# Kernel optimization log

Hardware: AMD Instinct MI355X
Metric: run time of the kernel (lower is better)

Reference implementation:

```python
import jax, jax.numpy as jnp
import numpy as np

NU, NI, E, D, B, L = 100000, 50000, 800000, 64, 1024, 2
P_DROP, TEMP = 0.25, 0.2
L1, L2, L3 = 0.2, 0.01, 1e-5


def setup_inputs() -> dict:
    k = jax.random.split(jax.random.key(0), 20)
    s = 0.02  # xavier-ish scale for embedding tables
    return dict(
        E_u_0=jax.random.normal(k[0], (NU, D), jnp.float32) * s,
        E_i_0=jax.random.normal(k[1], (NI, D), jnp.float32) * s,
        fuse_w=jax.random.normal(k[2], (E,), jnp.float32),
        fuse_b=jax.random.normal(k[3], (E,), jnp.float32),
        W1u=jax.random.normal(k[4], (D, D), jnp.float32) / np.sqrt(D),
        W1i=jax.random.normal(k[5], (D, D), jnp.float32) / np.sqrt(D),
        b1=jnp.zeros((D,), jnp.float32),
        W2=jax.random.normal(k[6], (D,), jnp.float32) / np.sqrt(D),
        b2=jnp.zeros((1,), jnp.float32),
        att_a=jax.random.normal(k[7], (2 * D,), jnp.float32) / np.sqrt(2 * D),
        wv_param=jax.random.normal(k[8], (E,), jnp.float32),
        Wg=jax.random.normal(k[9], (D, D), jnp.float32) / np.sqrt(D),
        adj_vals=jax.random.uniform(k[10], (E,), jnp.float32, 0.001, 0.02),
        drop_main_u=jax.random.uniform(k[11], (2 * L, E), jnp.float32),
        drop_aug_u=jax.random.uniform(k[12], (2 * L, E), jnp.float32),
        edge_src=jax.random.randint(k[13], (E,), 0, NU),
        edge_dst=jax.random.randint(k[14], (E,), 0, NI),
        uids=jax.random.randint(k[15], (B,), 0, NU),
        iids=jax.random.randint(k[16], (B,), 0, NI),
        pos_ids=jax.random.randint(k[17], (B,), 0, NI),
        neg_ids=jax.random.randint(k[18], (B,), 0, NI),
    )


def _forward(E_u_0, E_i_0, fuse_w, fuse_b, W1u, W1i, b1, W2, b2, att_a,
             wv_param, Wg, adj_vals, drop_main_u, drop_aug_u,
             edge_src, edge_dst, uids, iids, pos_ids, neg_ids):
    dt = adj_vals.dtype

    def spmm_u(vals, Xi):  # A @ Xi -> [NU, D]
        return jax.ops.segment_sum(vals[:, None] * Xi[edge_dst], edge_src, num_segments=NU)

    def spmm_i(vals, Xu):  # A.T @ Xu -> [NI, D]
        return jax.ops.segment_sum(vals[:, None] * Xu[edge_src], edge_dst, num_segments=NI)

    def mask(u):  # sparse_dropout: keep w.p. 1-p, rescale
        return (u > P_DROP).astype(dt) / (1.0 - P_DROP)

    def propagate(vals, drops):  # LightGCN-style sum over layers
        Eu, Ei = E_u_0, E_i_0
        Su, Si = Eu, Ei
        for layer in range(L):
            Eu_n = spmm_u(vals * mask(drops[2 * layer]), Ei)
            Ei_n = spmm_i(vals * mask(drops[2 * layer + 1]), Eu)
            Eu, Ei = Eu_n, Ei_n
            Su, Si = Su + Eu, Si + Ei
        return Su, Si

    E_u, E_i = propagate(adj_vals, drop_main_u)

    eu0, ei0 = E_u_0[edge_src], E_i_0[edge_dst]  # [E, D]
    # MLP view
    h = jax.nn.relu(eu0 @ W1u + ei0 @ W1i + b1)
    Ag_mlp = jax.nn.sigmoid(h @ W2 + b2[0])
    # WV view: learnable per-edge weight
    Ag_wv = jax.nn.sigmoid(wv_param)
    # GCN view: one propagation on current embeddings, bilinear edge score
    h_u = spmm_u(adj_vals, E_i)
    h_i = spmm_i(adj_vals, E_u)
    Ag_gcn = jax.nn.sigmoid(jnp.sum((h_u[edge_src] @ Wg) * h_i[edge_dst], axis=1))
    # ATT view: GAT-style
    Ag_att = jax.nn.sigmoid(jax.nn.leaky_relu(eu0 @ att_a[:D] + ei0 @ att_a[D:], 0.2))

    views = jnp.stack([Ag_mlp, Ag_wv, Ag_gcn, Ag_att])  # [4, E]
    w = jax.nn.softmax(jnp.tanh(fuse_w * views + fuse_b), axis=1)  # softmax over edges (as in source)
    Ag = jnp.sum(w * views, axis=0)
    Ag = (Ag + (views - Ag).sum(0)) / 5.0  # mlp_cof = 1 -> (sum(views) - 3*Ag) / 5

    # refine: sigmoid of endpoint dot products
    pre = jax.nn.sigmoid(jnp.sum(E_u[edge_src] * E_i[edge_dst], axis=1))
    baew = pre * Ag  # batch_aug_edge_weight

    aug_vals = jax.lax.stop_gradient(baew) * adj_vals  # new_graph * adj_norm (detach + Hadamard)
    Z_u, Z_i = propagate(aug_vals, drop_aug_u)

    # contrastive loss
    Gu, Gi = Z_u[uids], Z_i[iids]
    neg_sc = jnp.log(jnp.exp(Gu @ E_u.T / TEMP).sum(1) + 1e-8).mean() \
           + jnp.log(jnp.exp(Gi @ E_i.T / TEMP).sum(1) + 1e-8).mean()
    pos_sc = jnp.clip((Gu * E_u[uids]).sum(1) / TEMP, -5.0, 5.0).mean() \
           + jnp.clip((Gi * E_i[iids]).sum(1) / TEMP, -5.0, 5.0).mean()
    loss_cl = -pos_sc + neg_sc

    # BPR loss
    u_e, p_e, n_e = E_u[uids], E_i[pos_ids], E_i[neg_ids]
    diff = (u_e * p_e).sum(-1) - (u_e * n_e).sum(-1)
    loss_bpr = -jnp.log(jax.nn.sigmoid(diff)).mean()

    loss_pr = L2 * (-jnp.log(baew)).mean()

    params = [E_u_0, E_i_0, fuse_w, fuse_b, W1u, W1i, b1, W2, b2, att_a, wv_param, Wg]
    loss_reg = L3 * sum((p_ ** 2).sum() for p_ in params)

    loss = loss_bpr + L1 * loss_cl + loss_pr + loss_reg
    return loss, loss_bpr, L1 * loss_cl, loss_pr


def reference(E_u_0, E_i_0, fuse_w, fuse_b, W1u, W1i, b1, W2, b2, att_a,
              wv_param, Wg, adj_vals, drop_main_u, drop_aug_u,
              edge_src, edge_dst, uids, iids, pos_ids, neg_ids):
    return _forward(E_u_0, E_i_0, fuse_w, fuse_b, W1u, W1i, b1, W2, b2, att_a,
                    wv_param, Wg, adj_vals, drop_main_u, drop_aug_u,
                    edge_src, edge_dst, uids, iids, pos_ids, neg_ids)
```

## Files before the change

### kernel.cpp

```cpp
#include <hip/hip_runtime.h>
#include <math.h>

constexpr int NUc = 100000;
constexpr int NIc = 50000;
constexpr int Ec  = 800000;
constexpr int Bc  = 1024;

typedef __attribute__((ext_vector_type(8))) short short8;
typedef __attribute__((ext_vector_type(8))) unsigned short ushort8;
typedef __attribute__((ext_vector_type(4))) unsigned short ushort4v;
typedef __attribute__((ext_vector_type(4))) float floatx4;

__device__ __forceinline__ float sigf(float x) { return 1.f / (1.f + __expf(-x)); }
__device__ __forceinline__ float maskf(float u) { return (u > 0.25f) ? (1.f / 0.75f) : 0.f; }
__device__ __forceinline__ unsigned short f2bf(float f) {
    unsigned int u = __float_as_uint(f);
    unsigned int r = (u + 0x7fffu + ((u >> 16) & 1u)) >> 16;
    return (unsigned short)r;
}
__device__ __forceinline__ float bf2f(unsigned short u) {
    return __uint_as_float((unsigned int)u << 16);
}

__global__ void hist_k(const int* __restrict__ idx, int* __restrict__ cnt, int n) {
    int i = blockIdx.x * blockDim.x + threadIdx.x;
    if (i < n) atomicAdd(&cnt[idx[i]], 1);
}

__global__ void scan_block(const int* __restrict__ cnt, int* __restrict__ rp,
                           int* __restrict__ bsum, int N) {
    __shared__ int sh[1024];
    int i = blockIdx.x * 1024 + threadIdx.x;
    int v = (i < N) ? cnt[i] : 0;
    sh[threadIdx.x] = v;
    __syncthreads();
    for (int off = 1; off < 1024; off <<= 1) {
        int t = (threadIdx.x >= off) ? sh[threadIdx.x - off] : 0;
        __syncthreads();
        sh[threadIdx.x] += t;
        __syncthreads();
    }
    if (i < N) rp[i + 1] = sh[threadIdx.x];
    if (threadIdx.x == 1023) bsum[blockIdx.x] = sh[1023];
}

__global__ void scan_bsums(int* __restrict__ bsum, int nb) {
    __shared__ int sh[128];
    int t = threadIdx.x;
    int v = (t < nb) ? bsum[t] : 0;
    sh[t] = v;
    __syncthreads();
    for (int off = 1; off < 128; off <<= 1) {
        int x = (t >= off) ? sh[t - off] : 0;
        __syncthreads();
        sh[t] += x;
        __syncthreads();
    }
    if (t < nb) bsum[t] = sh[t] - v;
}

__global__ void scan_add(const int* __restrict__ bsum, int* __restrict__ rp, int N) {
    int i = blockIdx.x * blockDim.x + threadIdx.x;
    if (i == 0) rp[0] = 0;
    if (i < N) rp[i + 1] += bsum[i >> 10];
}

__global__ void fill_csr(const int* __restrict__ key, const int* __restrict__ other,
                         int* __restrict__ cur, int* __restrict__ col,
                         int* __restrict__ pos, int* __restrict__ perm, int n) {
    int i = blockIdx.x * blockDim.x + threadIdx.x;
    if (i < n) {
        int r = key[i];
        int p = atomicAdd(&cur[r], 1);
        col[p] = other[i];
        pos[i] = p;
        perm[p] = i;
    }
}

__global__ void build_rowu(const int* __restrict__ rp, int* __restrict__ rowu, int N) {
    int r = blockIdx.x * blockDim.x + threadIdx.x;
    if (r < N) {
        int s = rp[r], e = rp[r + 1];
        for (int p = s; p < e; ++p) rowu[p] = r;
    }
}

__global__ void build_w_gather(const int* __restrict__ perm, const float* __restrict__ vals,
                               const float* __restrict__ dA, const float* __restrict__ dB,
                               float* __restrict__ outA, float* __restrict__ outB, int E) {
    int p = blockIdx.x * blockDim.x + threadIdx.x;
    if (p >= E) return;
    int e = perm[p];
    float a = vals[e];
    outA[p] = a * maskf(dA[e]);
    outB[p] = a * maskf(dB[e]);
}

__global__ void gather_vals(const int* __restrict__ perm, const float* __restrict__ vals,
                            float* __restrict__ outA, int E) {
    int p = blockIdx.x * blockDim.x + threadIdx.x;
    if (p >= E) return;
    outA[p] = vals[perm[p]];
}

__global__ void spmm_bf(const int* __restrict__ rp, const int* __restrict__ col,
                        const float* __restrict__ w, const unsigned short* __restrict__ Xbf,
                        float* __restrict__ Acc, const float* __restrict__ Base,
                        unsigned short* __restrict__ Ybf, int ystride, int yoff, int N) {
    int row = blockIdx.x * (blockDim.x >> 6) + (threadIdx.x >> 6);
    int lane = threadIdx.x & 63;
    if (row >= N) return;
    int s = rp[row], e = rp[row + 1];
    float acc = 0.f;
    int j = s;
    for (; j + 4 <= e; j += 4) {
        int c0 = col[j], c1 = col[j + 1], c2 = col[j + 2], c3 = col[j + 3];
        float w0 = w[j], w1 = w[j + 1], w2 = w[j + 2], w3 = w[j + 3];
        float x0 = bf2f(Xbf[(size_t)c0 * 64 + lane]);
        float x1 = bf2f(Xbf[(size_t)c1 * 64 + lane]);
        float x2 = bf2f(Xbf[(size_t)c2 * 64 + lane]);
        float x3 = bf2f(Xbf[(size_t)c3 * 64 + lane]);
        acc = fmaf(w0, x0, acc);
        acc = fmaf(w1, x1, acc);
        acc = fmaf(w2, x2, acc);
        acc = fmaf(w3, x3, acc);
    }
    for (; j < e; ++j) acc = fmaf(w[j], bf2f(Xbf[(size_t)col[j] * 64 + lane]), acc);
    size_t o = (size_t)row * 64 + lane;
    if (Acc) Acc[o] = (Base ? Base[o] : Acc[o]) + acc;
    if (Ybf) Ybf[(size_t)row * ystride + yoff + lane] = f2bf(acc);
}

__global__ void gemm_n64_bf(const unsigned short* __restrict__ Xbf, const float* __restrict__ W,
                            unsigned short* __restrict__ P, int ostride, int ooff, int N) {
    __shared__ float Wl[64 * 64];
    for (int i = threadIdx.x; i < 4096; i += blockDim.x) Wl[i] = W[i];
    __syncthreads();
    int wid = blockIdx.x * (blockDim.x >> 6) + (threadIdx.x >> 6);
    int lane = threadIdx.x & 63;
    for (int r = 0; r < 8; ++r) {
        int row = wid * 8 + r;
        if (row >= N) break;
        const unsigned short* xr = Xbf + (size_t)row * 64;
        float acc = 0.f;
#pragma unroll
        for (int k = 0; k < 64; ++k) acc = fmaf(bf2f(xr[k]), Wl[k * 64 + lane], acc);
        P[(size_t)row * ostride + ooff + lane] = f2bf(acc);
    }
}

__global__ void rowdot64(const float* __restrict__ X, const float* __restrict__ a,
                         float* __restrict__ out, int N) {
    int wid = blockIdx.x * (blockDim.x >> 6) + (threadIdx.x >> 6);
    int lane = threadIdx.x & 63;
    float av = a[lane];
    for (int r = 0; r < 8; ++r) {
        int row = wid * 8 + r;
        if (row >= N) break;
        float v = X[(size_t)row * 64 + lane] * av;
#pragma unroll
        for (int off = 32; off; off >>= 1) v += __shfl_xor(v, off, 64);
        if (lane == 0) out[row] = v;
    }
}

__global__ void cvt_bf16(const float4* __restrict__ X, ushort4* __restrict__ Y, int n4) {
    int i = blockIdx.x * blockDim.x + threadIdx.x;
    if (i < n4) {
        float4 v = X[i];
        Y[i] = make_ushort4(f2bf(v.x), f2bf(v.y), f2bf(v.z), f2bf(v.w));
    }
}

__global__ void cvt_pack4(const float4* __restrict__ X, unsigned short* __restrict__ P,
                          int ostride, int ooff, int N) {
    int t = blockIdx.x * blockDim.x + threadIdx.x;
    if (t >= N * 16) return;
    int node = t >> 4, q = t & 15;
    float4 v = X[t];
    ushort4* dst = (ushort4*)(P + (size_t)node * ostride + ooff);
    dst[q] = make_ushort4(f2bf(v.x), f2bf(v.y), f2bf(v.z), f2bf(v.w));
}

__global__ void pack_bf4(const ushort4* __restrict__ X, unsigned short* __restrict__ P,
                         int ostride, int ooff, int N) {
    int t = blockIdx.x * blockDim.x + threadIdx.x;
    if (t >= N * 16) return;
    int node = t >> 4, q = t & 15;
    ((ushort4*)(P + (size_t)node * ostride + ooff))[q] = X[t];
}

__global__ void __launch_bounds__(128) edge_pass1(
        const int* __restrict__ rowu, const int* __restrict__ colP,
        const unsigned short* __restrict__ PU, const unsigned short* __restrict__ PI,
        const float* __restrict__ b1, const float* __restrict__ W2,
        const float* __restrict__ b2,
        const float* __restrict__ auv, const float* __restrict__ aiv,
        float4* __restrict__ vp4, int E) {
    __shared__ ushort4v lds4[128 * 49];
    int p0 = blockIdx.x * 128;
    int tid = threadIdx.x;
#pragma unroll
    for (int it = 0; it < 24; ++it) {
        int flat = it * 128 + tid;
        int row = flat / 24, c = flat - row * 24;
        int d = colP[p0 + row];
        ushort8 g = *(const ushort8*)(PI + (size_t)d * 192 + c * 8);
        ushort4v lo = {g[0], g[1], g[2], g[3]};
        ushort4v hi = {g[4], g[5], g[6], g[7]};
        lds4[row * 49 + c * 2]     = lo;
        lds4[row * 49 + c * 2 + 1] = hi;
    }
    __syncthreads();
    int p = p0 + tid;
    int s = rowu[p];
    int d = colP[p];
    const ushort8* pu = (const ushort8*)(PU + (size_t)s * 192);
    const ushort4v* pl = lds4 + tid * 49;
    float r1 = 0.f, r2 = 0.f, r3 = 0.f;
#pragma unroll
    for (int k = 0; k < 8; ++k) {
        ushort8 u1 = pu[k], hu = pu[8 + k], su = pu[16 + k];
// ... 59 lines not shown
        atomicAdd(&sumexp[threadIdx.x],
                  sh[0][threadIdx.x] + sh[1][threadIdx.x] + sh[2][threadIdx.x] + sh[3][threadIdx.x]);
}

__global__ void edge_pass2b(const float4* __restrict__ viewsE, const float* __restrict__ preE,
                            const float* __restrict__ fw, const float* __restrict__ fb,
                            const float* __restrict__ adj, const float* __restrict__ sumexp,
                            float* __restrict__ av, float* __restrict__ neglog, int E) {
    int e = blockIdx.x * blockDim.x + threadIdx.x;
    float nl = 0.f;
    if (e < E) {
        float s0 = sumexp[0], s1 = sumexp[1], s2 = sumexp[2], s3 = sumexp[3];
        float4 v = viewsE[e];
        float fwe = fw[e], fbe = fb[e];
        float w0 = __expf(tanhf(fmaf(fwe, v.x, fbe))) / s0;
        float w1 = __expf(tanhf(fmaf(fwe, v.y, fbe))) / s1;
        float w2 = __expf(tanhf(fmaf(fwe, v.z, fbe))) / s2;
        float w3 = __expf(tanhf(fmaf(fwe, v.w, fbe))) / s3;
        float agw = w0 * v.x + w1 * v.y + w2 * v.z + w3 * v.w;
        float sv = v.x + v.y + v.z + v.w;
        float Ag = (sv - 3.f * agw) * 0.2f;
        float bw = preE[e] * Ag;
        av[e] = bw * adj[e];
        nl = -logf(bw);
    }
#pragma unroll
    for (int off = 32; off; off >>= 1) nl += __shfl_xor(nl, off, 64);
    __shared__ float sh4[4];
    if ((threadIdx.x & 63) == 0) sh4[threadIdx.x >> 6] = nl;
    __syncthreads();
    if (threadIdx.x == 0) atomicAdd(neglog, sh4[0] + sh4[1] + sh4[2] + sh4[3]);
}

__global__ void gather_cvt(const float* __restrict__ X, const int* __restrict__ ids,
                           unsigned short* __restrict__ Y, int B_) {
    int t = blockIdx.x * blockDim.x + threadIdx.x;
    if (t >= B_ * 64) return;
    int b = t >> 6, k = t & 63;
    Y[t] = f2bf(X[(size_t)ids[b] * 64 + k]);
}

__global__ void lse_mfma(const unsigned short* __restrict__ Gbf,
                         const unsigned short* __restrict__ Ebf,
                         float* __restrict__ sums, int N, int tilesPerChunk) {
    int wid = blockIdx.x * (blockDim.x >> 6) + (threadIdx.x >> 6);
    int lane = threadIdx.x & 63;
    int bgroup = wid & 15;
    int chunk = wid >> 4;
    int ntiles = N >> 4;
    int t0 = chunk * tilesPerChunk;
    if (t0 >= ntiles) return;
    int t1 = t0 + tilesPerChunk; if (t1 > ntiles) t1 = ntiles;
    int m = lane & 15, quad = lane >> 4;

    short8 a0[4], a1[4];
#pragma unroll
    for (int t = 0; t < 4; ++t) {
        const short8* ap = (const short8*)(Gbf + ((size_t)(bgroup * 64 + t * 16 + m)) * 64 + quad * 8);
        a0[t] = ap[0];
        a1[t] = ap[4];
    }
    floatx4 rs[4];
#pragma unroll
    for (int t = 0; t < 4; ++t) rs[t] = (floatx4){0.f, 0.f, 0.f, 0.f};

    for (int jt = t0; jt < t1; ++jt) {
        const short8* bp = (const short8*)(Ebf + ((size_t)(jt * 16 + m)) * 64 + quad * 8);
        short8 bf0 = bp[0], bf1 = bp[4];
#pragma unroll
        for (int t = 0; t < 4; ++t) {
            floatx4 c = (floatx4){0.f, 0.f, 0.f, 0.f};
            c = __builtin_amdgcn_mfma_f32_16x16x32_bf16(a0[t], bf0, c, 0, 0, 0);
            c = __builtin_amdgcn_mfma_f32_16x16x32_bf16(a1[t], bf1, c, 0, 0, 0);
#pragma unroll
            for (int r = 0; r < 4; ++r) rs[t][r] += __expf(c[r] * 5.f);
        }
    }
#pragma unroll
    for (int t = 0; t < 4; ++t) {
#pragma unroll
        for (int r = 0; r < 4; ++r) {
            float v = rs[t][r];
            v += __shfl_xor(v, 1, 64);
            v += __shfl_xor(v, 2, 64);
            v += __shfl_xor(v, 4, 64);
            v += __shfl_xor(v, 8, 64);
            if (m == 0) atomicAdd(&sums[bgroup * 64 + t * 16 + quad * 4 + r], v);
        }
    }
}

__global__ void sumsq(const float* __restrict__ x, int n, float* __restrict__ acc) {
    float s = 0.f;
    for (int i = blockIdx.x * blockDim.x + threadIdx.x; i < n; i += gridDim.x * blockDim.x) {
        float v = x[i];
        s = fmaf(v, v, s);
    }
#pragma unroll
    for (int off = 32; off; off >>= 1) s += __shfl_xor(s, off, 64);
    __shared__ float sh[4];
    if ((threadIdx.x & 63) == 0) sh[threadIdx.x >> 6] = s;
    __syncthreads();
    if (threadIdx.x == 0) atomicAdd(acc, sh[0] + sh[1] + sh[2] + sh[3]);
}

__global__ void batch_partial(const float* __restrict__ Su, const float* __restrict__ Si,
                              const float* __restrict__ Zu, const float* __restrict__ Zi,
                              const int* __restrict__ uids, const int* __restrict__ iids,
                              const int* __restrict__ pids, const int* __restrict__ nids,
                              float* __restrict__ pos_b, float* __restrict__ bpr_b) {
    int b = blockIdx.x * (blockDim.x >> 6) + (threadIdx.x >> 6);
    if (b >= Bc) return;
    int lane = threadIdx.x & 63;
    int u = uids[b], ii = iids[b], p = pids[b], n = nids[b];
    float zu = Zu[(size_t)u * 64 + lane],  su = Su[(size_t)u * 64 + lane];
    float zi = Zi[(size_t)ii * 64 + lane], si = Si[(size_t)ii * 64 + lane];
    float pe = Si[(size_t)p * 64 + lane],  ne = Si[(size_t)n * 64 + lane];
    float du = zu * su, di = zi * si, dp = su * pe, dn = su * ne;
#pragma unroll
    for (int off = 32; off; off >>= 1) {
        du += __shfl_xor(du, off, 64);
        di += __shfl_xor(di, off, 64);
        dp += __shfl_xor(dp, off, 64);
        dn += __shfl_xor(dn, off, 64);
    }
    if (lane == 0) {
        pos_b[b] = fminf(fmaxf(du * 5.f, -5.f), 5.f) + fminf(fmaxf(di * 5.f, -5.f), 5.f);
        bpr_b[b] = log1pf(__expf(-(dp - dn)));
    }
}

__global__ void finalize_kernel(const float* __restrict__ sumexp_u, const float* __restrict__ sumexp_i,
                                const float* __restrict__ pos_b, const float* __restrict__ bpr_b,
                                const float* __restrict__ neglog, const float* __restrict__ regsum,
                                float* __restrict__ out) {
    int b = threadIdx.x;
    float lse = logf(sumexp_u[b] + 1e-8f) + logf(sumexp_i[b] + 1e-8f);
    float pos = pos_b[b];
    float bpr = bpr_b[b];
#pragma unroll
    for (int off = 32; off; off >>= 1) {
        lse += __shfl_xor(lse, off, 64);
        pos += __shfl_xor(pos, off, 64);
        bpr += __shfl_xor(bpr, off, 64);
    }
    __shared__ float sl[16], sp[16], sb[16];
    int w = b >> 6;
    if ((b & 63) == 0) { sl[w] = lse; sp[w] = pos; sb[w] = bpr; }
    __syncthreads();
    if (b == 0) {
        float L = 0.f, P = 0.f, Bz = 0.f;
        for (int i = 0; i < 16; ++i) { L += sl[i]; P += sp[i]; Bz += sb[i]; }
        float neg_sc = L * (1.f / Bc);
        float pos_sc = P * (1.f / Bc);
        float loss_cl = neg_sc - pos_sc;
        float l1cl = 0.2f * loss_cl;
        float loss_bpr = Bz * (1.f / Bc);
        float loss_pr = 0.01f * (neglog[0] * (1.f / Ec));
        float loss_reg = 1e-5f * regsum[0];
        out[0] = loss_bpr + l1cl + loss_pr + loss_reg;
        out[1] = loss_bpr;
        out[2] = l1cl;
// ... 39 lines not shown
    char* blkZ = alloc((size_t)NUc * 64 * 4 + (size_t)NIc * 64 * 4);
    unsigned short* PU = (unsigned short*)blkZ;
    float4* viewsE = (float4*)blkZ;
    float* preE   = (float*)(blkZ + (size_t)Ec * 16);
    float* Zu = (float*)blkZ;
    float* Zi = (float*)(blkZ + (size_t)NUc * 64 * 4);
    float4* vp4 = (float4*)alloc((size_t)Ec * 16);
    unsigned short* Eu0bf = (unsigned short*)alloc((size_t)NUc * 64 * 2);
    unsigned short* Ei0bf = (unsigned short*)alloc((size_t)NIc * 64 * 2);
    unsigned short* Subf  = (unsigned short*)alloc((size_t)NUc * 64 * 2);
    unsigned short* Sibf  = (unsigned short*)alloc((size_t)NIc * 64 * 2);
    unsigned short* Bubf  = (unsigned short*)alloc((size_t)NUc * 64 * 2);
    unsigned short* Bibf  = (unsigned short*)alloc((size_t)NIc * 64 * 2);
    unsigned short* hubf  = (unsigned short*)alloc((size_t)NUc * 64 * 2);
    unsigned short* hibf  = (unsigned short*)alloc((size_t)NIc * 64 * 2);
    char* blkA = alloc((size_t)Ec * 4 * 6);
    float* adjPu = (float*)blkA;
    float* adjPi = (float*)(blkA + (size_t)Ec * 4);
    float* wAu0  = (float*)(blkA + (size_t)Ec * 8);
    float* wAu1  = (float*)(blkA + (size_t)Ec * 12);
    float* wAi0  = (float*)(blkA + (size_t)Ec * 16);
    float* wAi1  = (float*)(blkA + (size_t)Ec * 20);
    unsigned short* PI = (unsigned short*)blkA;
    float* wMu0  = (float*)alloc((size_t)Ec * 4);
    float* wMu1  = (float*)alloc((size_t)Ec * 4);
    float* wMi0  = (float*)alloc((size_t)Ec * 4);
    float* wMi1  = (float*)alloc((size_t)Ec * 4);
    float* av    = (float*)alloc((size_t)Ec * 4);
    float* auv  = (float*)alloc((size_t)NUc * 4);
    float* aiv  = (float*)alloc((size_t)NIc * 4);
    int* rowu  = (int*)alloc((size_t)Ec * 4);
    unsigned short* Gubf = (unsigned short*)alloc((size_t)Bc * 64 * 2);
    unsigned short* Gibf = (unsigned short*)alloc((size_t)Bc * 64 * 2);
    float* sumexp4 = (float*)alloc(4 * 4);
    float* neglog  = (float*)alloc(4);
    float* regsum  = (float*)alloc(4);
    float* sumexp_u= (float*)alloc((size_t)Bc * 4);
    float* sumexp_i= (float*)alloc((size_t)Bc * 4);
    float* pos_b   = (float*)alloc((size_t)Bc * 4);
    float* bpr_b   = (float*)alloc((size_t)Bc * 4);
    int* rpu   = (int*)alloc((size_t)(NUc + 1) * 4);
    int* rpi   = (int*)alloc((size_t)(NIc + 1) * 4);
    int* colu  = (int*)alloc((size_t)Ec * 4);
    int* coli  = (int*)alloc((size_t)Ec * 4);
    int* posu  = (int*)alloc((size_t)Ec * 4);
    int* posi  = (int*)alloc((size_t)Ec * 4);
    int* permu = (int*)alloc((size_t)Ec * 4);
    int* permi = (int*)alloc((size_t)Ec * 4);
    int* cnt   = (int*)alloc((size_t)NUc * 4);
    int* cur   = (int*)alloc((size_t)NUc * 4);
    int* bsum  = (int*)alloc(128 * 4);

    dim3 b256(256);
    const int nbU = (NUc + 1023) / 1024;
    const int nbI = (NIc + 1023) / 1024;
    const dim3 gE((Ec + 255) / 256);
    const dim3 gU((NUc + 3) / 4), gI((NIc + 3) / 4);
    const dim3 gU8((NUc + 31) / 32), gI8((NIc + 31) / 32);
    const dim3 gUp((NUc * 16 + 255) / 256), gIp((NIc * 16 + 255) / 256);

    hipMemsetAsync(cnt, 0, (size_t)NUc * 4, stream);
    hist_k<<<gE, b256, 0, stream>>>(esrc, cnt, Ec);
    scan_block<<<dim3(nbU), dim3(1024), 0, stream>>>(cnt, rpu, bsum, NUc);
    scan_bsums<<<dim3(1), dim3(128), 0, stream>>>(bsum, nbU);
    scan_add<<<dim3((NUc + 255) / 256), b256, 0, stream>>>(bsum, rpu, NUc);
    hipMemcpyAsync(cur, rpu, (size_t)NUc * 4, hipMemcpyDeviceToDevice, stream);
    fill_csr<<<gE, b256, 0, stream>>>(esrc, edst, cur, colu, posu, permu, Ec);
    build_rowu<<<dim3((NUc + 255) / 256), b256, 0, stream>>>(rpu, rowu, NUc);

    hipMemsetAsync(cnt, 0, (size_t)NIc * 4, stream);
    hist_k<<<gE, b256, 0, stream>>>(edst, cnt, Ec);
    scan_block<<<dim3(nbI), dim3(1024), 0, stream>>>(cnt, rpi, bsum, NIc);
    scan_bsums<<<dim3(1), dim3(128), 0, stream>>>(bsum, nbI);
    scan_add<<<dim3((NIc + 255) / 256), b256, 0, stream>>>(bsum, rpi, NIc);
    hipMemcpyAsync(cur, rpi, (size_t)NIc * 4, hipMemcpyDeviceToDevice, stream);
    fill_csr<<<gE, b256, 0, stream>>>(edst, esrc, cur, coli, posi, permi, Ec);

    build_w_gather<<<gE, b256, 0, stream>>>(permu, adj, dmain, dmain + 2 * (size_t)Ec, wMu0, wMu1, Ec);
    build_w_gather<<<gE, b256, 0, stream>>>(permi, adj, dmain + (size_t)Ec, dmain + 3 * (size_t)Ec, wMi0, wMi1, Ec);
    gather_vals<<<gE, b256, 0, stream>>>(permu, adj, adjPu, Ec);
    gather_vals<<<gE, b256, 0, stream>>>(permi, adj, adjPi, Ec);

    cvt_bf16<<<gUp, b256, 0, stream>>>((const float4*)Eu0, (ushort4*)Eu0bf, NUc * 16);
    cvt_bf16<<<gIp, b256, 0, stream>>>((const float4*)Ei0, (ushort4*)Ei0bf, NIc * 16);

    spmm_bf<<<gU, b256, 0, stream>>>(rpu, colu, wMu0, Ei0bf, Su, Eu0, Bubf, 64, 0, NUc);
    spmm_bf<<<gI, b256, 0, stream>>>(rpi, coli, wMi0, Eu0bf, Si, Ei0, Bibf, 64, 0, NIc);
    spmm_bf<<<gU, b256, 0, stream>>>(rpu, colu, wMu1, Bibf, Su, nullptr, nullptr, 64, 0, NUc);
    spmm_bf<<<gI, b256, 0, stream>>>(rpi, coli, wMi1, Bubf, Si, nullptr, nullptr, 64, 0, NIc);

    cvt_bf16<<<gUp, b256, 0, stream>>>((const float4*)Su, (ushort4*)Subf, NUc * 16);
    cvt_bf16<<<gIp, b256, 0, stream>>>((const float4*)Si, (ushort4*)Sibf, NIc * 16);

    spmm_bf<<<gU, b256, 0, stream>>>(rpu, colu, adjPu, Sibf, nullptr, nullptr, hubf, 64, 0, NUc);
    spmm_bf<<<gI, b256, 0, stream>>>(rpi, coli, adjPi, Subf, nullptr, nullptr, hibf, 64, 0, NIc);
    gemm_n64_bf<<<gU8, b256, 0, stream>>>(hubf, Wg, PU, 192, 64, NUc);
    gemm_n64_bf<<<gU8, b256, 0, stream>>>(Eu0bf, W1u, PU, 192, 0, NUc);
    gemm_n64_bf<<<gI8, b256, 0, stream>>>(Ei0bf, W1i, PI, 192, 0, NIc);
    pack_bf4<<<gIp, b256, 0, stream>>>((const ushort4*)hibf, PI, 192, 64, NIc);
    cvt_pack4<<<gUp, b256, 0, stream>>>((const float4*)Su, PU, 192, 128, NUc);
    cvt_pack4<<<gIp, b256, 0, stream>>>((const float4*)Si, PI, 192, 128, NIc);

    rowdot64<<<gU8, b256, 0, stream>>>(Eu0, att, auv, NUc);
    rowdot64<<<gI8, b256, 0, stream>>>(Ei0, att + 64, aiv, NIc);

    edge_pass1<<<dim3(Ec / 128), dim3(128), 0, stream>>>(
        rowu, colu, PU, PI, b1, W2, b2, auv, aiv, vp4, Ec);

    hipMemsetAsync(sumexp4, 0, 4 * 4, stream);
    edge_pass2a<<<gE, b256, 0, stream>>>(vp4, posu, fuse_w, fuse_b, wv,
                                         viewsE, preE, sumexp4, Ec);

    hipMemsetAsync(neglog, 0, 4, stream);
    edge_pass2b<<<gE, b256, 0, stream>>>(
        viewsE, preE, fuse_w, fuse_b, adj, sumexp4, av, neglog, Ec);

    build_w_gather<<<gE, b256, 0, stream>>>(permu, av, daug, daug + 2 * (size_t)Ec, wAu0, wAu1, Ec);
    build_w_gather<<<gE, b256, 0, stream>>>(permi, av, daug + (size_t)Ec, daug + 3 * (size_t)Ec, wAi0, wAi1, Ec);

    spmm_bf<<<gU, b256, 0, stream>>>(rpu, colu, wAu0, Ei0bf, Zu, Eu0, Bubf, 64, 0, NUc);
    spmm_bf<<<gI, b256, 0, stream>>>(rpi, coli, wAi0, Eu0bf, Zi, Ei0, Bibf, 64, 0, NIc);
    spmm_bf<<<gU, b256, 0, stream>>>(rpu, colu, wAu1, Bibf, Zu, nullptr, nullptr, 64, 0, NUc);
    spmm_bf<<<gI, b256, 0, stream>>>(rpi, coli, wAi1, Bubf, Zi, nullptr, nullptr, 64, 0, NIc);

    gather_cvt<<<dim3((Bc * 64 + 255) / 256), b256, 0, stream>>>(Zu, uids, Gubf, Bc);
    gather_cvt<<<dim3((Bc * 64 + 255) / 256), b256, 0, stream>>>(Zi, iids, Gibf, Bc);
    hipMemsetAsync(sumexp_u, 0, (size_t)Bc * 4, stream);
    hipMemsetAsync(sumexp_i, 0, (size_t)Bc * 4, stream);
    lse_mfma<<<dim3(640), b256, 0, stream>>>(Gubf, Subf, sumexp_u, NUc, 40);
    lse_mfma<<<dim3(320), b256, 0, stream>>>(Gibf, Sibf, sumexp_i, NIc, 40);

    batch_partial<<<dim3(Bc / 4), b256, 0, stream>>>(Su, Si, Zu, Zi, uids, iids, pids, nids,
                                                     pos_b, bpr_b);

    hipMemsetAsync(regsum, 0, 4, stream);
    auto ss = [&](const float* p, int n) {
        int g = (n + 2047) / 2048;
        if (g > 1024) g = 1024;
        if (g < 1) g = 1;
        sumsq<<<dim3(g), b256, 0, stream>>>(p, n, regsum);
    };
    ss(Eu0, NUc * 64); ss(Ei0, NIc * 64); ss(fuse_w, Ec); ss(fuse_b, Ec);
    ss(W1u, 4096); ss(W1i, 4096); ss(b1, 64); ss(W2, 64); ss(b2, 1);
    ss(att, 128); ss(wv, Ec); ss(Wg, 4096);

    finalize_kernel<<<dim3(1), dim3(1024), 0, stream>>>(
        sumexp_u, sumexp_i, pos_b, bpr_b, neglog, regsum, out);
}
```

Measured before the change: 1.368 ms.

## Merge user/item kernel pairs and fuse prep stages to cut launch count

Builds both CSR structures from one histogram, one scan and one fill pass, and merges the user and item SpMM, weight-build, conversion, gather and log-sum-exp kernels into single launches that split work by block index. The two GEMMs, the attention row-dots and the packing into PU/PI are folded into per-side prep kernels, and bf16 copies of Su/Si are written inside the SpMM. The twelve sumsq launches and several memsets are collapsed into one kernel and one memset. The aim is to cut launch overhead and redundant memory passes, at the cost of larger kernels with more shared memory per block in prep_PU.

After: 1.253 ms. 8.4% less time.

```diff
diff --git a/kernel.cpp b/kernel.cpp
--- a/kernel.cpp
+++ b/kernel.cpp
@@ -22,12 +22,16 @@
     return __uint_as_float((unsigned int)u << 16);
 }
 
-__global__ void hist_k(const int* __restrict__ idx, int* __restrict__ cnt, int n) {
+__global__ void hist_both(const int* __restrict__ esrc, const int* __restrict__ edst,
+                          int* __restrict__ cntAll, int n) {
     int i = blockIdx.x * blockDim.x + threadIdx.x;
-    if (i < n) atomicAdd(&cnt[idx[i]], 1);
-}
-
-__global__ void scan_block(const int* __restrict__ cnt, int* __restrict__ rp,
+    if (i < n) {
+        atomicAdd(&cntAll[esrc[i]], 1);
+        atomicAdd(&cntAll[NUc + edst[i]], 1);
+    }
+}
+
+__global__ void scan_block(const int* __restrict__ cnt, int* __restrict__ scanAll,
                            int* __restrict__ bsum, int N) {
     __shared__ int sh[1024];
     int i = blockIdx.x * 1024 + threadIdx.x;
@@ -40,17 +44,17 @@
         sh[threadIdx.x] += t;
         __syncthreads();
     }
-    if (i < N) rp[i + 1] = sh[threadIdx.x];
+    if (i < N) scanAll[i] = sh[threadIdx.x];
     if (threadIdx.x == 1023) bsum[blockIdx.x] = sh[1023];
 }
 
 __global__ void scan_bsums(int* __restrict__ bsum, int nb) {
-    __shared__ int sh[128];
+    __shared__ int sh[256];
     int t = threadIdx.x;
     int v = (t < nb) ? bsum[t] : 0;
     sh[t] = v;
     __syncthreads();
-    for (int off = 1; off < 128; off <<= 1) {
+    for (int off = 1; off < 256; off <<= 1) {
         int x = (t >= off) ? sh[t - off] : 0;
         __syncthreads();
         sh[t] += x;
@@ -59,23 +63,36 @@
     if (t < nb) bsum[t] = sh[t] - v;
 }
 
-__global__ void scan_add(const int* __restrict__ bsum, int* __restrict__ rp, int N) {
+__global__ void scan_add_cur(const int* __restrict__ scanAll, const int* __restrict__ bsum,
+                             const int* __restrict__ cnt,
+                             int* __restrict__ rpu, int* __restrict__ rpi,
+                             int* __restrict__ curu, int* __restrict__ curi) {
     int i = blockIdx.x * blockDim.x + threadIdx.x;
-    if (i == 0) rp[0] = 0;
-    if (i < N) rp[i + 1] += bsum[i >> 10];
-}
-
-__global__ void fill_csr(const int* __restrict__ key, const int* __restrict__ other,
-                         int* __restrict__ cur, int* __restrict__ col,
-                         int* __restrict__ pos, int* __restrict__ perm, int n) {
+    if (i >= NUc + NIc) return;
+    int v = scanAll[i] + bsum[i >> 10];
+    if (i < NUc) {
+        rpu[i + 1] = v;
+        if (i == 0) rpu[0] = 0;
+        curu[i] = v - cnt[i];
+    } else {
+        int j = i - NUc;
+        rpi[j + 1] = v - Ec;
+        if (j == 0) rpi[0] = 0;
+        curi[j] = v - Ec - cnt[i];
+    }
+}
+
+__global__ void fill_both(const int* __restrict__ esrc, const int* __restrict__ edst,
+                          int* __restrict__ curu, int* __restrict__ curi,
+                          int* __restrict__ colu, int* __restrict__ posu, int* __restrict__ permu,
+                          int* __restrict__ coli, int* __restrict__ permi, int n) {
     int i = blockIdx.x * blockDim.x + threadIdx.x;
-    if (i < n) {
-        int r = key[i];
-        int p = atomicAdd(&cur[r], 1);
-        col[p] = other[i];
-        pos[i] = p;
-        perm[p] = i;
-    }
+    if (i >= n) return;
+    int s = esrc[i], d = edst[i];
+    int pu = atomicAdd(&curu[s], 1);
+    colu[pu] = d; posu[i] = pu; permu[pu] = i;
+    int pi = atomicAdd(&curi[d], 1);
+    coli[pi] = s; permi[pi] = i;
 }
 
 __global__ void build_rowu(const int* __restrict__ rp, int* __restrict__ rowu, int N) {
@@ -86,31 +103,54 @@
     }
 }
 
-__global__ void build_w_gather(const int* __restrict__ perm, const float* __restrict__ vals,
-                               const float* __restrict__ dA, const float* __restrict__ dB,
-                               float* __restrict__ outA, float* __restrict__ outB, int E) {
+__global__ void build_w_main_both(const int* __restrict__ permu, const int* __restrict__ permi,
+                                  const float* __restrict__ adj, const float* __restrict__ dmain,
+                                  float* __restrict__ wMu0, float* __restrict__ wMu1,
+                                  float* __restrict__ adjPu,
+                                  float* __restrict__ wMi0, float* __restrict__ wMi1,
+                                  float* __restrict__ adjPi) {
     int p = blockIdx.x * blockDim.x + threadIdx.x;
-    if (p >= E) return;
-    int e = perm[p];
-    float a = vals[e];
-    outA[p] = a * maskf(dA[e]);
-    outB[p] = a * maskf(dB[e]);
-}
-
-__global__ void gather_vals(const int* __restrict__ perm, const float* __restrict__ vals,
-                            float* __restrict__ outA, int E) {
+    if (p < Ec) {
+        int e = permu[p];
+        float a = adj[e];
+        wMu0[p] = a * maskf(dmain[e]);
+        wMu1[p] = a * maskf(dmain[2 * (size_t)Ec + e]);
+        adjPu[p] = a;
+    } else if (p < 2 * Ec) {
+        p -= Ec;
+        int e = permi[p];
+        float a = adj[e];
+        wMi0[p] = a * maskf(dmain[(size_t)Ec + e]);
+        wMi1[p] = a * maskf(dmain[3 * (size_t)Ec + e]);
+        adjPi[p] = a;
+    }
+}
+
+__global__ void build_w_aug_both(const int* __restrict__ permu, const int* __restrict__ permi,
+                                 const float* __restrict__ av, const float* __restrict__ daug,
+                                 float* __restrict__ wAu0, float* __restrict__ wAu1,
+                                 float* __restrict__ wAi0, float* __restrict__ wAi1) {
     int p = blockIdx.x * blockDim.x + threadIdx.x;
-    if (p >= E) return;
-    outA[p] = vals[perm[p]];
-}
-
-__global__ void spmm_bf(const int* __restrict__ rp, const int* __restrict__ col,
-                        const float* __restrict__ w, const unsigned short* __restrict__ Xbf,
-                        float* __restrict__ Acc, const float* __restrict__ Base,
-                        unsigned short* __restrict__ Ybf, int ystride, int yoff, int N) {
-    int row = blockIdx.x * (blockDim.x >> 6) + (threadIdx.x >> 6);
-    int lane = threadIdx.x & 63;
-    if (row >= N) return;
+    if (p < Ec) {
+        int e = permu[p];
+        float a = av[e];
+        wAu0[p] = a * maskf(daug[e]);
+        wAu1[p] = a * maskf(daug[2 * (size_t)Ec + e]);
+    } else if (p < 2 * Ec) {
+        p -= Ec;
+        int e = permi[p];
+        float a = av[e];
+        wAi0[p] = a * maskf(daug[(size_t)Ec + e]);
+        wAi1[p] = a * maskf(daug[3 * (size_t)Ec + e]);
+    }
+}
+
+__device__ __forceinline__ void spmm_core(
+        const int* __restrict__ rp, const int* __restrict__ col,
+        const float* __restrict__ w, const unsigned short* __restrict__ Xbf,
+        float* __restrict__ Acc, const float* __restrict__ Base,
+        unsigned short* __restrict__ Ybf, unsigned short* __restrict__ Accbf,
+        int row, int lane) {
     int s = rp[row], e = rp[row + 1];
     float acc = 0.f;
     int j = s;
@@ -128,67 +168,110 @@
     }
     for (; j < e; ++j) acc = fmaf(w[j], bf2f(Xbf[(size_t)col[j] * 64 + lane]), acc);
     size_t o = (size_t)row * 64 + lane;
-    if (Acc) Acc[o] = (Base ? Base[o] : Acc[o]) + acc;
-    if (Ybf) Ybf[(size_t)row * ystride + yoff + lane] = f2bf(acc);
-}
-
-__global__ void gemm_n64_bf(const unsigned short* __restrict__ Xbf, const float* __restrict__ W,
-                            unsigned short* __restrict__ P, int ostride, int ooff, int N) {
-    __shared__ float Wl[64 * 64];
-    for (int i = threadIdx.x; i < 4096; i += blockDim.x) Wl[i] = W[i];
+    if (Acc) {
+        float nv = (Base ? Base[o] : Acc[o]) + acc;
+        Acc[o] = nv;
+        if (Accbf) Accbf[o] = f2bf(nv);
+    }
+    if (Ybf) Ybf[o] = f2bf(acc);
+}
+
+__global__ void spmm_bf2(int blocksA,
+        const int* __restrict__ rpA, const int* __restrict__ colA, const float* __restrict__ wA,
+        const unsigned short* __restrict__ XA, float* __restrict__ AccA,
+        const float* __restrict__ BaseA, unsigned short* __restrict__ YA,
+        unsigned short* __restrict__ AbfA, int NA,
+        const int* __restrict__ rpB, const int* __restrict__ colB, const float* __restrict__ wB,
+        const unsigned short* __restrict__ XB, float* __restrict__ AccB,
+        const float* __restrict__ BaseB, unsigned short* __restrict__ YB,
+        unsigned short* __restrict__ AbfB, int NB) {
+    int lane = threadIdx.x & 63;
+    int w4 = threadIdx.x >> 6;
+    int bx = blockIdx.x;
+    if (bx < blocksA) {
+        int row = bx * 4 + w4;
+        if (row < NA) spmm_core(rpA, colA, wA, XA, AccA, BaseA, YA, AbfA, row, lane);
+    } else {
+        int row = (bx - blocksA) * 4 + w4;
+        if (row < NB) spmm_core(rpB, colB, wB, XB, AccB, BaseB, YB, AbfB, row, lane);
+    }
+}
+
+__global__ void prep_PU(const unsigned short* __restrict__ Eu0bf,
+                        const unsigned short* __restrict__ hubf,
+                        const unsigned short* __restrict__ Subf,
+                        const float* __restrict__ W1, const float* __restrict__ Wg,
+                        const float* __restrict__ att,
+                        unsigned short* __restrict__ PU, float* __restrict__ auv, int N) {
+    __shared__ float W1l[4096];
+    __shared__ float Wgl[4096];
+    for (int i = threadIdx.x; i < 4096; i += blockDim.x) { W1l[i] = W1[i]; Wgl[i] = Wg[i]; }
     __syncthreads();
     int wid = blockIdx.x * (blockDim.x >> 6) + (threadIdx.x >> 6);
     int lane = threadIdx.x & 63;
     for (int r = 0; r < 8; ++r) {
         int row = wid * 8 + r;
         if (row >= N) break;
-        const unsigned short* xr = Xbf + (size_t)row * 64;
-        float acc = 0.f;
-#pragma unroll
-        for (int k = 0; k < 64; ++k) acc = fmaf(bf2f(xr[k]), Wl[k * 64 + lane], acc);
-        P[(size_t)row * ostride + ooff + lane] = f2bf(acc);
-    }
-}
-
-__global__ void rowdot64(const float* __restrict__ X, const float* __restrict__ a,
-                         float* __restrict__ out, int N) {
+        const unsigned short* xr = Eu0bf + (size_t)row * 64;
+        const unsigned short* hr = hubf + (size_t)row * 64;
+        float a1 = 0.f, a2 = 0.f, ad = 0.f;
+#pragma unroll
+        for (int k = 0; k < 64; ++k) {
+            float xv = bf2f(xr[k]);
+            a1 = fmaf(xv, W1l[k * 64 + lane], a1);
+            a2 = fmaf(bf2f(hr[k]), Wgl[k * 64 + lane], a2);
+            ad = fmaf(xv, att[k], ad);
+        }
+        size_t base = (size_t)row * 192;
+        PU[base + lane]       = f2bf(a1);
+        PU[base + 64 + lane]  = f2bf(a2);
+        PU[base + 128 + lane] = Subf[(size_t)row * 64 + lane];
+        if (lane == 0) auv[row] = ad;
+    }
+}
+
+__global__ void prep_PI(const unsigned short* __restrict__ Ei0bf,
+                        const unsigned short* __restrict__ hibf,
+                        const unsigned short* __restrict__ Sibf,
+                        const float* __restrict__ W1, const float* __restrict__ att,
+                        unsigned short* __restrict__ PI, float* __restrict__ aiv, int N) {
+    __shared__ float W1l[4096];
+    for (int i = threadIdx.x; i < 4096; i += blockDim.x) W1l[i] = W1[i];
+    __syncthreads();
     int wid = blockIdx.x * (blockDim.x >> 6) + (threadIdx.x >> 6);
     int lane = threadIdx.x & 63;
-    float av = a[lane];
     for (int r = 0; r < 8; ++r) {
         int row = wid * 8 + r;
         if (row >= N) break;
-        float v = X[(size_t)row * 64 + lane] * av;
-#pragma unroll
-        for (int off = 32; off; off >>= 1) v += __shfl_xor(v, off, 64);
-        if (lane == 0) out[row] = v;
-    }
-}
-
-__global__ void cvt_bf16(const float4* __restrict__ X, ushort4* __restrict__ Y, int n4) {
+        const unsigned short* xr = Ei0bf + (size_t)row * 64;
+        float a1 = 0.f, ad = 0.f;
+#pragma unroll
+        for (int k = 0; k < 64; ++k) {
+            float xv = bf2f(xr[k]);
+            a1 = fmaf(xv, W1l[k * 64 + lane], a1);
+            ad = fmaf(xv, att[k], ad);
+        }
+        size_t base = (size_t)row * 192;
+        PI[base + lane]       = f2bf(a1);
+        PI[base + 64 + lane]  = hibf[(size_t)row * 64 + lane];
+        PI[base + 128 + lane] = Sibf[(size_t)row * 64 + lane];
+        if (lane == 0) aiv[row] = ad;
+    }
+}
+
+__global__ void cvt_both(const float4* __restrict__ Xu, ushort4* __restrict__ Yu, int n4u,
+                         const float4* __restrict__ Xi, ushort4* __restrict__ Yi, int n4i) {
     int i = blockIdx.x * blockDim.x + threadIdx.x;
-    if (i < n4) {
-        float4 v = X[i];
-        Y[i] = make_ushort4(f2bf(v.x), f2bf(v.y), f2bf(v.z), f2bf(v.w));
-    }
-}
-
-__global__ void cvt_pack4(const float4* __restrict__ X, unsigned short* __restrict__ P,
-                          int ostride, int ooff, int N) {
-    int t = blockIdx.x * blockDim.x + threadIdx.x;
-    if (t >= N * 16) return;
-    int node = t >> 4, q = t & 15;
-    float4 v = X[t];
-    ushort4* dst = (ushort4*)(P + (size_t)node * ostride + ooff);
-    dst[q] = make_ushort4(f2bf(v.x), f2bf(v.y), f2bf(v.z), f2bf(v.w));
-}
-
-__global__ void pack_bf4(const ushort4* __restrict__ X, unsigned short* __restrict__ P,
-                         int ostride, int ooff, int N) {
-    int t = blockIdx.x * blockDim.x + threadIdx.x;
-    if (t >= N * 16) return;
-    int node = t >> 4, q = t & 15;
-    ((ushort4*)(P + (size_t)node * ostride + ooff))[q] = X[t];
+    if (i < n4u) {
+        float4 v = Xu[i];
+        Yu[i] = make_ushort4(f2bf(v.x), f2bf(v.y), f2bf(v.z), f2bf(v.w));
+    } else {
+        i -= n4u;
+        if (i < n4i) {
+            float4 v = Xi[i];
+            Yi[i] = make_ushort4(f2bf(v.x), f2bf(v.y), f2bf(v.z), f2bf(v.w));
+        }
+    }
 }
 
 __global__ void __launch_bounds__(128) edge_pass1(
@@ -314,19 +397,23 @@
     if (threadIdx.x == 0) atomicAdd(neglog, sh4[0] + sh4[1] + sh4[2] + sh4[3]);
 }
 
-__global__ void gather_cvt(const float* __restrict__ X, const int* __restrict__ ids,
-                           unsigned short* __restrict__ Y, int B_) {
+__global__ void gather_cvt_both(const float* __restrict__ Zu, const int* __restrict__ uids,
+                                unsigned short* __restrict__ Gu,
+                                const float* __restrict__ Zi, const int* __restrict__ iids,
+                                unsigned short* __restrict__ Gi) {
     int t = blockIdx.x * blockDim.x + threadIdx.x;
-    if (t >= B_ * 64) return;
-    int b = t >> 6, k = t & 63;
-    Y[t] = f2bf(X[(size_t)ids[b] * 64 + k]);
-}
-
-__global__ void lse_mfma(const unsigned short* __restrict__ Gbf,
-                         const unsigned short* __restrict__ Ebf,
-                         float* __restrict__ sums, int N, int tilesPerChunk) {
-    int wid = blockIdx.x * (blockDim.x >> 6) + (threadIdx.x >> 6);
-    int lane = threadIdx.x & 63;
+    if (t < Bc * 64) {
+        Gu[t] = f2bf(Zu[(size_t)uids[t >> 6] * 64 + (t & 63)]);
+    } else {
+        t -= Bc * 64;
+        if (t < Bc * 64) Gi[t] = f2bf(Zi[(size_t)iids[t >> 6] * 64 + (t & 63)]);
+    }
+}
+
+__device__ __forceinline__ void lse_core(const unsigned short* __restrict__ Gbf,
+                                         const unsigned short* __restrict__ Ebf,
+                                         float* __restrict__ sums, int N, int tilesPerChunk,
+                                         int wid, int lane) {
     int bgroup = wid & 15;
     int chunk = wid >> 4;
     int ntiles = N >> 4;
@@ -372,18 +459,17 @@
     }
 }
 
-__global__ void sumsq(const float* __restrict__ x, int n, float* __restrict__ acc) {
-    float s = 0.f;
-    for (int i = blockIdx.x * blockDim.x + threadIdx.x; i < n; i += gridDim.x * blockDim.x) {
-        float v = x[i];
-        s = fmaf(v, v, s);
-    }
-#pragma unroll
-    for (int off = 32; off; off >>= 1) s += __shfl_xor(s, off, 64);
-    __shared__ float sh[4];
-    if ((threadIdx.x & 63) == 0) sh[threadIdx.x >> 6] = s;
-    __syncthreads();
-    if (threadIdx.x == 0) atomicAdd(acc, sh[0] + sh[1] + sh[2] + sh[3]);
+__global__ void lse_both(const unsigned short* __restrict__ Gu, const unsigned short* __restrict__ Su,
+                         float* __restrict__ sums_u,
+                         const unsigned short* __restrict__ Gi, const unsigned short* __restrict__ Si,
+                         float* __restrict__ sums_i) {
+    int lane = threadIdx.x & 63;
+    int w4 = threadIdx.x >> 6;
+    if ((int)blockIdx.x < 640) {
+        lse_core(Gu, Su, sums_u, NUc, 40, blockIdx.x * 4 + w4, lane);
+    } else {
+        lse_core(Gi, Si, sums_i, NIc, 40, (blockIdx.x - 640) * 4 + w4, lane);
+    }
 }
 
 __global__ void batch_partial(const float* __restrict__ Su, const float* __restrict__ Si,
@@ -410,6 +496,41 @@
         pos_b[b] = fminf(fmaxf(du * 5.f, -5.f), 5.f) + fminf(fmaxf(di * 5.f, -5.f), 5.f);
         bpr_b[b] = log1pf(__expf(-(dp - dn)));
     }
+}
+
+__global__ void sumsq_all(const float* __restrict__ p0, const float* __restrict__ p1,
+                          const float* __restrict__ p2, const float* __restrict__ p3,
+                          const float* __restrict__ p4, const float* __restrict__ p5,
+                          const float* __restrict__ p6, const float* __restrict__ p7,
+                          const float* __restrict__ p8, const float* __restrict__ p9,
+                          const float* __restrict__ p10, const float* __restrict__ p11,
+                          float* __restrict__ acc) {
+    const int TOT = 6400000 + 3200000 + 3 * 800000 + 3 * 4096 + 128 + 64 + 64 + 1;
+    float s = 0.f;
+    for (int t = blockIdx.x * blockDim.x + threadIdx.x; t < TOT; t += gridDim.x * blockDim.x) {
+        int i = t;
+        const float* P;
+        if (i < 6400000) P = p0;
+        else if ((i -= 6400000) < 3200000) P = p1;
+        else if ((i -= 3200000) < 800000) P = p2;
+        else if ((i -= 800000) < 800000) P = p3;
+        else if ((i -= 800000) < 800000) P = p4;
+        else if ((i -= 800000) < 4096) P = p5;
+        else if ((i -= 4096) < 4096) P = p6;
+        else if ((i -= 4096) < 4096) P = p7;
+        else if ((i -= 4096) < 128) P = p8;
+        else if ((i -= 128) < 64) P = p9;
+        else if ((i -= 64) < 64) P = p10;
+        else { i -= 64; P = p11; }
+        float v = P[i];
+        s = fmaf(v, v, s);
+    }
+#pragma unroll
+    for (int off = 32; off; off >>= 1) s += __shfl_xor(s, off, 64);
+    __shared__ float sh[4];
+    if ((threadIdx.x & 63) == 0) sh[threadIdx.x >> 6] = s;
+    __syncthreads();
+    if (threadIdx.x == 0) atomicAdd(acc, sh[0] + sh[1] + sh[2] + sh[3]);
 }
 
 __global__ void finalize_kernel(const float* __restrict__ sumexp_u, const float* __restrict__ sumexp_i,
@@ -515,117 +636,95 @@
     int* rowu  = (int*)alloc((size_t)Ec * 4);
     unsigned short* Gubf = (unsigned short*)alloc((size_t)Bc * 64 * 2);
     unsigned short* Gibf = (unsigned short*)alloc((size_t)Bc * 64 * 2);
-    float* sumexp4 = (float*)alloc(4 * 4);
-    float* neglog  = (float*)alloc(4);
-    float* regsum  = (float*)alloc(4);
-    float* sumexp_u= (float*)alloc((size_t)Bc * 4);
-    float* sumexp_i= (float*)alloc((size_t)Bc * 4);
-    float* pos_b   = (float*)alloc((size_t)Bc * 4);
-    float* bpr_b   = (float*)alloc((size_t)Bc * 4);
+    float* scal = (float*)alloc((4 + 1 + 1 + 2 + Bc + Bc) * 4);
+    float* sumexp4 = scal;
+    float* neglog  = scal + 4;
+    float* regsum  = scal + 5;
+    float* sumexp_u = scal + 8;
+    float* sumexp_i = scal + 8 + Bc;
+    float* pos_b = (float*)alloc((size_t)Bc * 4);
+    float* bpr_b = (float*)alloc((size_t)Bc * 4);
     int* rpu   = (int*)alloc((size_t)(NUc + 1) * 4);
     int* rpi   = (int*)alloc((size_t)(NIc + 1) * 4);
     int* colu  = (int*)alloc((size_t)Ec * 4);
     int* coli  = (int*)alloc((size_t)Ec * 4);
     int* posu  = (int*)alloc((size_t)Ec * 4);
-    int* posi  = (int*)alloc((size_t)Ec * 4);
     int* permu = (int*)alloc((size_t)Ec * 4);
     int* permi = (int*)alloc((size_t)Ec * 4);
-    int* cnt   = (int*)alloc((size_t)NUc * 4);
-    int* cur   = (int*)alloc((size_t)NUc * 4);
-    int* bsum  = (int*)alloc(128 * 4);
+    int* cntAll  = (int*)alloc((size_t)(NUc + NIc) * 4);
+    int* scanAll = (int*)alloc((size_t)(NUc + NIc) * 4);
+    int* curu  = (int*)alloc((size_t)NUc * 4);
+    int* curi  = (int*)alloc((size_t)NIc * 4);
+    int* bsum  = (int*)alloc(256 * 4);
 
     dim3 b256(256);
-    const int nbU = (NUc + 1023) / 1024;
-    const int nbI = (NIc + 1023) / 1024;
+    const int NALL = NUc + NIc;
+    const int nbAll = (NALL + 1023) / 1024;
     const dim3 gE((Ec + 255) / 256);
-    const dim3 gU((NUc + 3) / 4), gI((NIc + 3) / 4);
+    const dim3 g2E((2 * Ec + 255) / 256);
+    const int blocksU = (NUc + 3) / 4, blocksI = (NIc + 3) / 4;
+    const dim3 gUI(blocksU + blocksI);
     const dim3 gU8((NUc + 31) / 32), gI8((NIc + 31) / 32);
-    const dim3 gUp((NUc * 16 + 255) / 256), gIp((NIc * 16 + 255) / 256);
-
-    hipMemsetAsync(cnt, 0, (size_t)NUc * 4, stream);
-    hist_k<<<gE, b256, 0, stream>>>(esrc, cnt, Ec);
-    scan_block<<<dim3(nbU), dim3(1024), 0, stream>>>(cnt, rpu, bsum, NUc);
-    scan_bsums<<<dim3(1), dim3(128), 0, stream>>>(bsum, nbU);
-    scan_add<<<dim3((NUc + 255) / 256), b256, 0, stream>>>(bsum, rpu, NUc);
-    hipMemcpyAsync(cur, rpu, (size_t)NUc * 4, hipMemcpyDeviceToDevice, stream);
-    fill_csr<<<gE, b256, 0, stream>>>(esrc, edst, cur, colu, posu, permu, Ec);
+
+    hipMemsetAsync(cntAll, 0, (size_t)NALL * 4, stream);
+    hipMemsetAsync(scal, 0, (4 + 1 + 1 + 2 + Bc + Bc) * 4, stream);
+
+    hist_both<<<gE, b256, 0, stream>>>(esrc, edst, cntAll, Ec);
+    scan_block<<<dim3(nbAll), dim3(1024), 0, stream>>>(cntAll, scanAll, bsum, NALL);
+    scan_bsums<<<dim3(1), dim3(256), 0, stream>>>(bsum, nbAll);
+    scan_add_cur<<<dim3((NALL + 255) / 256), b256, 0, stream>>>(scanAll, bsum, cntAll,
+                                                               rpu, rpi, curu, curi);
+    fill_both<<<gE, b256, 0, stream>>>(esrc, edst, curu, curi, colu, posu, permu, coli, permi, Ec);
     build_rowu<<<dim3((NUc + 255) / 256), b256, 0, stream>>>(rpu, rowu, NUc);
 
-    hipMemsetAsync(cnt, 0, (size_t)NIc * 4, stream);
-    hist_k<<<gE, b256, 0, stream>>>(edst, cnt, Ec);
-    scan_block<<<dim3(nbI), dim3(1024), 0, stream>>>(cnt, rpi, bsum, NIc);
-    scan_bsums<<<dim3(1), dim3(128), 0, stream>>>(bsum, nbI);
-    scan_add<<<dim3((NIc + 255) / 256), b256, 0, stream>>>(bsum, rpi, NIc);
-    hipMemcpyAsync(cur, rpi, (size_t)NIc * 4, hipMemcpyDeviceToDevice, stream);
-    fill_csr<<<gE, b256, 0, stream>>>(edst, esrc, cur, coli, posi, permi, Ec);
-
-    build_w_gather<<<gE, b256, 0, stream>>>(permu, adj, dmain, dmain + 2 * (size_t)Ec, wMu0, wMu1, Ec);
-    build_w_gather<<<gE, b256, 0, stream>>>(permi, adj, dmain + (size_t)Ec, dmain + 3 * (size_t)Ec, wMi0, wMi1, Ec);
-    gather_vals<<<gE, b256, 0, stream>>>(permu, adj, adjPu, Ec);
-    gather_vals<<<gE, b256, 0, stream>>>(permi, adj, adjPi, Ec);
-
-    cvt_bf16<<<gUp, b256, 0, stream>>>((const float4*)Eu0, (ushort4*)Eu0bf, NUc * 16);
-    cvt_bf16<<<gIp, b256, 0, stream>>>((const float4*)Ei0, (ushort4*)Ei0bf, NIc * 16);
-
-    spmm_bf<<<gU, b256, 0, stream>>>(rpu, colu, wMu0, Ei0bf, Su, Eu0, Bubf, 64, 0, NUc);
-    spmm_bf<<<gI, b256, 0, stream>>>(rpi, coli, wMi0, Eu0bf, Si, Ei0, Bibf, 64, 0, NIc);
-    spmm_bf<<<gU, b256, 0, stream>>>(rpu, colu, wMu1, Bibf, Su, nullptr, nullptr, 64, 0, NUc);
-    spmm_bf<<<gI, b256, 0, stream>>>(rpi, coli, wMi1, Bubf, Si, nullptr, nullptr, 64, 0, NIc);
-
-    cvt_bf16<<<gUp, b256, 0, stream>>>((const float4*)Su, (ushort4*)Subf, NUc * 16);
-    cvt_bf16<<<gIp, b256, 0, stream>>>((const float4*)Si, (ushort4*)Sibf, NIc * 16);
-
-    spmm_bf<<<gU, b256, 0, stream>>>(rpu, colu, adjPu, Sibf, nullptr, nullptr, hubf, 64, 0, NUc);
-    spmm_bf<<<gI, b256, 0, stream>>>(rpi, coli, adjPi, Subf, nullptr, nullptr, hibf, 64, 0, NIc);
-    gemm_n64_bf<<<gU8, b256, 0, stream>>>(hubf, Wg, PU, 192, 64, NUc);
-    gemm_n64_bf<<<gU8, b256, 0, stream>>>(Eu0bf, W1u, PU, 192, 0, NUc);
-    gemm_n64_bf<<<gI8, b256, 0, stream>>>(Ei0bf, W1i, PI, 192, 0, NIc);
-    pack_bf4<<<gIp, b256, 0, stream>>>((const ushort4*)hibf, PI, 192, 64, NIc);
-    cvt_pack4<<<gUp, b256, 0, stream>>>((const float4*)Su, PU, 192, 128, NUc);
-    cvt_pack4<<<gIp, b256, 0, stream>>>((const float4*)Si, PI, 192, 128, NIc);
-
-    rowdot64<<<gU8, b256, 0, stream>>>(Eu0, att, auv, NUc);
-    rowdot64<<<gI8, b256, 0, stream>>>(Ei0, att + 64, aiv, NIc);
+    build_w_main_both<<<g2E, b256, 0, stream>>>(permu, permi, adj, dmain,
+                                                wMu0, wMu1, adjPu, wMi0, wMi1, adjPi);
+
+    cvt_both<<<dim3(((NUc + NIc) * 16 + 255) / 256), b256, 0, stream>>>(
+        (const float4*)Eu0, (ushort4*)Eu0bf, NUc * 16,
+        (const float4*)Ei0, (ushort4*)Ei0bf, NIc * 16);
+
+    spmm_bf2<<<gUI, b256, 0, stream>>>(blocksU,
+        rpu, colu, wMu0, Ei0bf, Su, Eu0, Bubf, nullptr, NUc,
+        rpi, coli, wMi0, Eu0bf, Si, Ei0, Bibf, nullptr, NIc);
+    spmm_bf2<<<gUI, b256, 0, stream>>>(blocksU,
+        rpu, colu, wMu1, Bibf, Su, nullptr, nullptr, Subf, NUc,
+        rpi, coli, wMi1, Bubf, Si, nullptr, nullptr, Sibf, NIc);
+
+    spmm_bf2<<<gUI, b256, 0, stream>>>(blocksU,
+        rpu, colu, adjPu, Sibf, nullptr, nullptr, hubf, nullptr, NUc,
+        rpi, coli, adjPi, Subf, nullptr, nullptr, hibf, nullptr, NIc);
+
+    prep_PU<<<gU8, b256, 0, stream>>>(Eu0bf, hubf, Subf, W1u, Wg, att, PU, auv, NUc);
+    prep_PI<<<gI8, b256, 0, stream>>>(Ei0bf, hibf, Sibf, W1i, att + 64, PI, aiv, NIc);
 
     edge_pass1<<<dim3(Ec / 128), dim3(128), 0, stream>>>(
         rowu, colu, PU, PI, b1, W2, b2, auv, aiv, vp4, Ec);
 
-    hipMemsetAsync(sumexp4, 0, 4 * 4, stream);
     edge_pass2a<<<gE, b256, 0, stream>>>(vp4, posu, fuse_w, fuse_b, wv,
                                          viewsE, preE, sumexp4, Ec);
 
-    hipMemsetAsync(neglog, 0, 4, stream);
     edge_pass2b<<<gE, b256, 0, stream>>>(
         viewsE, preE, fuse_w, fuse_b, adj, sumexp4, av, neglog, Ec);
 
-    build_w_gather<<<gE, b256, 0, stream>>>(permu, av, daug, daug + 2 * (size_t)Ec, wAu0, wAu1, Ec);
-    build_w_gather<<<gE, b256, 0, stream>>>(permi, av, daug + (size_t)Ec, daug + 3 * (size_t)Ec, wAi0, wAi1, Ec);
-
-    spmm_bf<<<gU, b256, 0, stream>>>(rpu, colu, wAu0, Ei0bf, Zu, Eu0, Bubf, 64, 0, NUc);
-    spmm_bf<<<gI, b256, 0, stream>>>(rpi, coli, wAi0, Eu0bf, Zi, Ei0, Bibf, 64, 0, NIc);
-    spmm_bf<<<gU, b256, 0, stream>>>(rpu, colu, wAu1, Bibf, Zu, nullptr, nullptr, 64, 0, NUc);
-    spmm_bf<<<gI, b256, 0, stream>>>(rpi, coli, wAi1, Bubf, Zi, nullptr, nullptr, 64, 0, NIc);
-
-    gather_cvt<<<dim3((Bc * 64 + 255) / 256), b256, 0, stream>>>(Zu, uids, Gubf, Bc);
-    gather_cvt<<<dim3((Bc * 64 + 255) / 256), b256, 0, stream>>>(Zi, iids, Gibf, Bc);
-    hipMemsetAsync(sumexp_u, 0, (size_t)Bc * 4, stream);
-    hipMemsetAsync(sumexp_i, 0, (size_t)Bc * 4, stream);
-    lse_mfma<<<dim3(640), b256, 0, stream>>>(Gubf, Subf, sumexp_u, NUc, 40);
-    lse_mfma<<<dim3(320), b256, 0, stream>>>(Gibf, Sibf, sumexp_i, NIc, 40);
+    build_w_aug_both<<<g2E, b256, 0, stream>>>(permu, permi, av, daug, wAu0, wAu1, wAi0, wAi1);
+
+    spmm_bf2<<<gUI, b256, 0, stream>>>(blocksU,
+        rpu, colu, wAu0, Ei0bf, Zu, Eu0, Bubf, nullptr, NUc,
+        rpi, coli, wAi0, Eu0bf, Zi, Ei0, Bibf, nullptr, NIc);
+    spmm_bf2<<<gUI, b256, 0, stream>>>(blocksU,
+        rpu, colu, wAu1, Bibf, Zu, nullptr, nullptr, nullptr, NUc,
+        rpi, coli, wAi1, Bubf, Zi, nullptr, nullptr, nullptr, NIc);
+
+    gather_cvt_both<<<dim3((2 * Bc * 64 + 255) / 256), b256, 0, stream>>>(
+        Zu, uids, Gubf, Zi, iids, Gibf);
+    lse_both<<<dim3(960), b256, 0, stream>>>(Gubf, Subf, sumexp_u, Gibf, Sibf, sumexp_i);
 
     batch_partial<<<dim3(Bc / 4), b256, 0, stream>>>(Su, Si, Zu, Zi, uids, iids, pids, nids,
                                                      pos_b, bpr_b);
 
-    hipMemsetAsync(regsum, 0, 4, stream);
-    auto ss = [&](const float* p, int n) {
-        int g = (n + 2047) / 2048;
-        if (g > 1024) g = 1024;
-        if (g < 1) g = 1;
-        sumsq<<<dim3(g), b256, 0, stream>>>(p, n, regsum);
-    };
-    ss(Eu0, NUc * 64); ss(Ei0, NIc * 64); ss(fuse_w, Ec); ss(fuse_b, Ec);
-    ss(W1u, 4096); ss(W1i, 4096); ss(b1, 64); ss(W2, 64); ss(b2, 1);
-    ss(att, 128); ss(wv, Ec); ss(Wg, 4096);
+    sumsq_all<<<dim3(4096), b256, 0, stream>>>(Eu0, Ei0, fuse_w, fuse_b, wv,
+                                               W1u, W1i, Wg, att, b1, W2, b2, regsum);
 
     finalize_kernel<<<dim3(1), dim3(1024), 0, stream>>>(
         sumexp_u, sumexp_i, pos_b, bpr_b, neglog, regsum, out);
```
